# Kernel tuning notes

Hardware: AMD Instinct MI355X
Metric: run time of the kernel (lower is better)

## Reference

```python
import jax, jax.numpy as jnp
import numpy as np
from jax import lax

B, CIN, H, W = 8, 256, 64, 64
CC = 128          # corr_channels
COUT = 64         # out_channels
KH = KW = 5       # corr_kernel_size
SH = SW = 1       # corr_stride
PT, PB = KH // 2, (KH + 1) // 2 - 1   # pad='k'
PL, PR = KW // 2, (KW + 1) // 2 - 1


def setup_inputs() -> dict:
    key = jax.random.key(0)
    k1, k2, k3, k4, k5 = jax.random.split(key, 5)
    x = jax.random.normal(k1, (B, CIN, H, W), dtype=jnp.float32)
    w_ext = jax.random.normal(k2, (CC, CIN, 3, 3), dtype=jnp.float32) * 0.02
    b_ext = jax.random.normal(k3, (CC,), dtype=jnp.float32) * 0.02
    w_reg = jax.random.normal(k4, (COUT, CC, KH, KW), dtype=jnp.float32) * 0.02
    b_reg = jax.random.normal(k5, (COUT,), dtype=jnp.float32) * 0.02
    return {"x": x, "w_ext": w_ext, "b_ext": b_ext, "w_reg": w_reg, "b_reg": b_reg}


def _forward(x, w_ext, b_ext, w_reg, b_reg):
    # feature extraction: 3x3 conv, padding 1
    f = lax.conv_general_dilated(x, w_ext, (1, 1), ((1, 1), (1, 1)))
    f = f + b_ext[None, :, None, None]
    # local autocorrelation: multiply each window element by the window center, per channel
    fp = jnp.pad(f, ((0, 0), (0, 0), (PT, PB), (PL, PR)))
    nH = (fp.shape[2] - KH) // SH + 1
    nW = (fp.shape[3] - KW) // SW + 1
    center = fp[:, :, KH // 2:KH // 2 + nH * SH:SH, KW // 2:KW // 2 + nW * SW:SW]  # [B,CC,nH,nW]
    patches = jnp.stack(
        [fp[:, :, u:u + nH * SH:SH, v:v + nW * SW:SW] for u in range(KH) for v in range(KW)],
        axis=-1)  # [B,CC,nH,nW,KH*KW]
    corr = patches * center[..., None]  # [B,CC,nH,nW,KH*KW]
    out = jnp.einsum('bcijk,ock->bijo', corr, w_reg.reshape(COUT, CC, KH * KW))
    out = out + b_reg
    return out.transpose(0, 3, 1, 2)  # permute=True -> [B, COUT, nH, nW]


def reference(x, w_ext, b_ext, w_reg, b_reg):
    return _forward(x, w_ext, b_ext, w_reg, b_reg)
```

## Files before the change

### kernel.cpp

```cpp
#include <hip/hip_runtime.h>
#include <hip/hip_bf16.h>

#define B_    8
#define CIN_  256
#define CC_   128
#define COUT_ 64
#define HP_   68
#define HPX_  (HP_ * HP_)
#define XQW_  66
#define XQPX_ (XQW_ * XQW_)

typedef __attribute__((ext_vector_type(8))) short bh8;
typedef __attribute__((ext_vector_type(4))) float f4;

__device__ __forceinline__ ushort f2bf(float f) {
    uint u = __float_as_uint(f);
    return (ushort)((u + 0x7fffu + ((u >> 16) & 1u)) >> 16);
}
__device__ __forceinline__ float bf2f(ushort s) {
    return __uint_as_float(((uint)s) << 16);
}
__device__ __forceinline__ short f2bf_c(float f) {
    __hip_bfloat16 h = __float2bfloat16(f);
    short s;
    __builtin_memcpy(&s, &h, 2);
    return s;
}

__global__ __launch_bounds__(256) void zero_ring(ushort* __restrict__ fpad_t) {
    int e = blockIdx.x * 256 + threadIdx.x;
    if (e >= 8 * 528 * 16) return;
    int seg = e & 15;
    int t = e >> 4;
    int b = t / 528, rp = t - b * 528;
    int i, j;
    if (rp < 136) { i = rp / 68; j = rp - (rp / 68) * 68; }
    else if (rp < 272) { int r = rp - 136; i = 66 + r / 68; j = r - (r / 68) * 68; }
    else { int r = rp - 272; i = 2 + (r >> 2); int c = r & 3; j = (c < 2) ? c : c + 64; }
    uint4 z; z.x = 0u; z.y = 0u; z.z = 0u; z.w = 0u;
    *(uint4*)&fpad_t[(((size_t)b * HPX_) + i * HP_ + j) * 128 + seg * 8] = z;
}

__global__ __launch_bounds__(256) void prep_x(const float* __restrict__ x,
                                              ushort* __restrict__ xq) {
    __shared__ float xt[2][32][65];
    const int tid = threadIdx.x;
    const int rp = blockIdx.x, cb = blockIdx.y, b = blockIdx.z;

#pragma unroll
    for (int rr = 0; rr < 2; ++rr) {
        int y = rp * 2 + rr - 1;
        if ((unsigned)y < 64u) {
            int xx = tid & 63, wv = tid >> 6;
#pragma unroll
            for (int it = 0; it < 8; ++it) {
                int ci = it * 4 + wv;
                xt[rr][ci][xx] = x[(((size_t)(b * CIN_ + cb * 32 + ci)) * 64 + y) * 64 + xx];
            }
        }
    }
    __syncthreads();

    for (int e = tid; e < 528; e += 256) {
        int rr = e / 264, t = e - rr * 264;
        int hc = t >> 2, seg = t & 3;
        int y = rp * 2 + rr - 1, xx = hc - 1;
        uint pk[4] = {0u, 0u, 0u, 0u};
        if ((unsigned)y < 64u && (unsigned)xx < 64u) {
#pragma unroll
            for (int i = 0; i < 4; ++i) {
                uint lo = f2bf(xt[rr][seg * 8 + i * 2][xx]);
                uint hi = f2bf(xt[rr][seg * 8 + i * 2 + 1][xx]);
                pk[i] = lo | (hi << 16);
            }
        }
        uint4 v; v.x = pk[0]; v.y = pk[1]; v.z = pk[2]; v.w = pk[3];
        *(uint4*)&xq[((((size_t)(b * 8 + cb)) * XQPX_) + (rp * 2 + rr) * XQW_ + hc) * 32 + seg * 8] = v;
    }
}

__global__ void prep_wext(const float* __restrict__ w, short* __restrict__ wg) {
    int e = blockIdx.x * 256 + threadIdx.x;
    if (e >= 8 * 9 * 128 * 32) return;
    int ci = e & 31;
    int t  = e >> 5;
    int cc = t & 127;
    int t2 = t >> 7;
    int rs = t2 % 9, cb = t2 / 9;
    wg[e] = (short)f2bf(w[(cc * CIN_ + cb * 32 + ci) * 9 + rs]);
}

__global__ void prep_wA(const float* __restrict__ w, short* __restrict__ wa) {
    int e = blockIdx.x * 256 + threadIdx.x;
    if (e >= 4 * 25 * 64 * 32) return;
    int ci = e & 31;
    int o  = (e >> 5) & 63;
    int rest = e >> 11;
    int k = rest % 25, q = rest / 25;
    wa[e] = (short)f2bf(w[(o * CC_ + q * 32 + ci) * 25 + k]);
}

__device__ __forceinline__ void stage_xq(const ushort* __restrict__ xq, short* __restrict__ dst,
                                         int b, int cb, int i0, int j0, int tid) {
    const ushort* base = xq + (((size_t)(b * 8 + cb)) * XQPX_) * 32;
    for (int e = tid; e < 400; e += 256) {
        int hp = e >> 2, seg = e & 3;
        int hr = hp / 10, hc = hp - hr * 10;
        const ushort* src = base + ((size_t)((i0 + hr) * XQW_ + (j0 + hc))) * 32 + seg * 8;
        *(bh8*)&dst[hp * 72 + seg * 8] = *(const bh8*)src;
    }
}

__global__ __launch_bounds__(256) void conv3x3_mfma(const ushort* __restrict__ xq,
                                                    const short* __restrict__ wg,
                                                    const float* __restrict__ bext,
                                                    ushort* __restrict__ fpad_t) {
    __shared__ __align__(16) short xh[2][100 * 72];
    const int tid = threadIdx.x;
    const int lane = tid & 63, wv = tid >> 6;
    const int j0 = blockIdx.x * 8, i0 = blockIdx.y * 8, b = blockIdx.z;
    const int l15 = lane & 15, kg = lane >> 4;
    const int cc0 = wv * 32;

    f4 acc[2][4] = {};

    stage_xq(xq, xh[0], b, 0, i0, j0, tid);
    __syncthreads();

    for (int cb = 0; cb < 8; ++cb) {
        const int buf = cb & 1;
        if (cb < 7) stage_xq(xq, xh[buf ^ 1], b, cb + 1, i0, j0, tid);

        const short* wbase = wg + (size_t)(cb * 9) * 128 * 32;
#pragma unroll
        for (int rs = 0; rs < 9; ++rs) {
            const int r = rs / 3, s = rs % 3;
            bh8 a[2], bb[4];
#pragma unroll
            for (int mm = 0; mm < 2; ++mm)
                a[mm] = *(const bh8*)(wbase + (rs * 128 + cc0 + mm * 16 + l15) * 32 + kg * 8);
#pragma unroll
            for (int nn = 0; nn < 4; ++nn) {
                int px = nn * 16 + l15, pi = px >> 3, pj = px & 7;
                int hidx = (pi + r) * 10 + (pj + s);
                bb[nn] = *(const bh8*)&xh[buf][hidx * 72 + kg * 8];
            }
#pragma unroll
            for (int mm = 0; mm < 2; ++mm)
#pragma unroll
                for (int nn = 0; nn < 4; ++nn)
                    acc[mm][nn] = __builtin_amdgcn_mfma_f32_16x16x32_bf16(
                        a[mm], bb[nn], acc[mm][nn], 0, 0, 0);
        }
        __syncthreads();
    }

#pragma unroll
    for (int mm = 0; mm < 2; ++mm) {
        const int ccb = cc0 + mm * 16 + kg * 4;
        float bv0 = bext[ccb + 0], bv1 = bext[ccb + 1];
        float bv2 = bext[ccb + 2], bv3 = bext[ccb + 3];
#pragma unroll
        for (int nn = 0; nn < 4; ++nn) {
            int px = nn * 16 + l15, pi = px >> 3, pj = px & 7;
            size_t row = (size_t)b * HPX_ + (2 + i0 + pi) * HP_ + (2 + j0 + pj);
            uint lo = (uint)f2bf(acc[mm][nn][0] + bv0) | ((uint)f2bf(acc[mm][nn][1] + bv1) << 16);
            uint hi = (uint)f2bf(acc[mm][nn][2] + bv2) | ((uint)f2bf(acc[mm][nn][3] + bv3) << 16);
            uint2 pk; pk.x = lo; pk.y = hi;
            *(uint2*)&fpad_t[row * 128 + ccb] = pk;
        }
    }
}

__global__ __launch_bounds__(256) void autocorr_mfma(const ushort* __restrict__ ft,
                                                     const short* __restrict__ wA,
                                                     const float* __restrict__ breg,
                                                     float* __restrict__ out) {
    __shared__ __align__(16) short flds[144 * 136];
    const int tid = threadIdx.x;
    const int lane = tid & 63, wv = tid >> 6;
    const int oh = wv >> 1, ph = wv & 1;
    const int j0 = blockIdx.x * 8, i0 = blockIdx.y * 8, b = blockIdx.z;
    const int l15 = lane & 15, kg = lane >> 4;

    for (int e = tid; e < 2304; e += 256) {
        int hp = e >> 4, seg = e & 15;
        int hr = hp / 12, hc = hp - hr * 12;
        const ushort* src = ft + ((size_t)b * HPX_ + (i0 + hr) * HP_ + (j0 + hc)) * 128 + seg * 8;
        *(bh8*)&flds[hp * 136 + seg * 8] = *(const bh8*)src;
    }
    __syncthreads();

    f4 acc[2][2] = {};
    int base_off[2], cen_off[2];
#pragma unroll
    for (int t = 0; t < 2; ++t) {
        int px = ph * 32 + t * 16 + l15;
        int pi = px >> 3, pj = px & 7;
        base_off[t] = (pi * 12 + pj) * 136 + kg * 8;
        cen_off[t]  = ((pi + 2) * 12 + (pj + 2)) * 136 + kg * 8;
    }

#pragma unroll 1
    for (int q = 0; q < 4; ++q) {
        float cen[2][8];
#pragma unroll
        for (int t = 0; t < 2; ++t) {
            bh8 c8 = *(const bh8*)&flds[cen_off[t] + q * 32];
#pragma unroll
            for (int jj = 0; jj < 8; ++jj) cen[t][jj] = bf2f((ushort)c8[jj]);
        }
        const short* wq = wA + q * (25 * 64 * 32);
#pragma unroll
        for (int k = 0; k < 25; ++k) {
            const int u = k / 5, v = k % 5;
            const int koff = (u * 12 + v) * 136;
            bh8 a[2];
#pragma unroll
            for (int mm = 0; mm < 2; ++mm)
                a[mm] = *(const bh8*)(wq + (k * 64 + oh * 32 + mm * 16 + l15) * 32 + kg * 8);
            bh8 bb[2];
#pragma unroll
            for (int t = 0; t < 2; ++t) {
                bh8 s8 = *(const bh8*)&flds[base_off[t] + q * 32 + koff];
#pragma unroll
                for (int jj = 0; jj < 8; ++jj) {
                    float p = bf2f((ushort)s8[jj]) * cen[t][jj];
                    bb[t][jj] = f2bf_c(p);
                }
            }
#pragma unroll
            for (int mm = 0; mm < 2; ++mm)
#pragma unroll
                for (int t = 0; t < 2; ++t)
                    acc[mm][t] = __builtin_amdgcn_mfma_f32_16x16x32_bf16(
                        a[mm], bb[t], acc[mm][t], 0, 0, 0);
        }
    }

#pragma unroll
    for (int mm = 0; mm < 2; ++mm) {
#pragma unroll
        for (int reg = 0; reg < 4; ++reg) {
            int o = oh * 32 + mm * 16 + kg * 4 + reg;
            float bv = breg[o];
#pragma unroll
            for (int t = 0; t < 2; ++t) {
                int px = ph * 32 + t * 16 + l15, pi = px >> 3, pj = px & 7;
                out[(((size_t)(b * COUT_ + o)) * 64 + i0 + pi) * 64 + j0 + pj] =
                    acc[mm][t][reg] + bv;
            }
        }
    }
}

extern "C" void kernel_launch(void* const* d_in, const int* in_sizes, int n_in,
                              void* d_out, int out_size, void* d_ws, size_t ws_size,
                              hipStream_t stream) {
    const float* x     = (const float*)d_in[0];
    const float* w_ext = (const float*)d_in[1];
    const float* b_ext = (const float*)d_in[2];
    const float* w_reg = (const float*)d_in[3];
    const float* b_reg = (const float*)d_in[4];
    float* out = (float*)d_out;

    char* ws = (char*)d_ws;
    const size_t FPADT_BYTES = (size_t)B_ * HPX_ * 128 * 2;
    const size_t WG_BYTES    = (size_t)8 * 9 * 128 * 32 * 2;
    const size_t WA_BYTES    = (size_t)4 * 25 * 64 * 32 * 2;
    ushort* fpad_t = (ushort*)ws;
    short*  wgq    = (short*)(ws + FPADT_BYTES);
    short*  wa     = (short*)(ws + FPADT_BYTES + WG_BYTES);
    ushort* xq     = (ushort*)(ws + FPADT_BYTES + WG_BYTES + WA_BYTES);

    zero_ring<<<(8 * 528 * 16 + 255) / 256, 256, 0, stream>>>(fpad_t);

    dim3 pgrid(33, 8, 8);
    prep_x<<<pgrid, 256, 0, stream>>>(x, xq);
    prep_wext<<<(8 * 9 * 128 * 32 + 255) / 256, 256, 0, stream>>>(w_ext, wgq);
    prep_wA<<<(4 * 25 * 64 * 32 + 255) / 256, 256, 0, stream>>>(w_reg, wa);

    dim3 grid(8, 8, 8);
    conv3x3_mfma<<<grid, 256, 0, stream>>>(xq, wgq, b_ext, fpad_t);
    autocorr_mfma<<<grid, 256, 0, stream>>>(fpad_t, wa, b_reg, out);
}
```

Baseline: 86.95 us.

## Drop LDS staging in conv and autocorr kernels, merge prep kernels

Both MFMA kernels stop staging input tiles into shared memory and instead have each lane read its B operand straight from global/L2. The work is re-split so each wave owns 16 pixels and all output channels, which removes the barriers and LDS traffic. In exchange, overlapping halo reads now go through the caches and each wave loads the full set of weight A fragments. The zero-ring and two weight-conversion kernels are also merged into one launch to cut launch overhead.

```diff
diff --git a/kernel.cpp b/kernel.cpp
--- a/kernel.cpp
+++ b/kernel.cpp
@@ -27,18 +27,42 @@
     return s;
 }
 
-__global__ __launch_bounds__(256) void zero_ring(ushort* __restrict__ fpad_t) {
+__global__ __launch_bounds__(256) void prep_misc(const float* __restrict__ w_ext,
+                                                 const float* __restrict__ w_reg,
+                                                 short* __restrict__ wg,
+                                                 short* __restrict__ wa,
+                                                 ushort* __restrict__ fpad_t) {
     int e = blockIdx.x * 256 + threadIdx.x;
-    if (e >= 8 * 528 * 16) return;
-    int seg = e & 15;
-    int t = e >> 4;
-    int b = t / 528, rp = t - b * 528;
-    int i, j;
-    if (rp < 136) { i = rp / 68; j = rp - (rp / 68) * 68; }
-    else if (rp < 272) { int r = rp - 136; i = 66 + r / 68; j = r - (r / 68) * 68; }
-    else { int r = rp - 272; i = 2 + (r >> 2); int c = r & 3; j = (c < 2) ? c : c + 64; }
-    uint4 z; z.x = 0u; z.y = 0u; z.z = 0u; z.w = 0u;
-    *(uint4*)&fpad_t[(((size_t)b * HPX_) + i * HP_ + j) * 128 + seg * 8] = z;
+    if (e < 67584) {
+        int seg = e & 15;
+        int t = e >> 4;
+        int b = t / 528, rp = t - b * 528;
+        int i, j;
+        if (rp < 136) { i = rp / 68; j = rp - (rp / 68) * 68; }
+        else if (rp < 272) { int r = rp - 136; i = 66 + r / 68; j = r - (r / 68) * 68; }
+        else { int r = rp - 272; i = 2 + (r >> 2); int c = r & 3; j = (c < 2) ? c : c + 64; }
+        uint4 z; z.x = 0u; z.y = 0u; z.z = 0u; z.w = 0u;
+        *(uint4*)&fpad_t[(((size_t)b * HPX_) + i * HP_ + j) * 128 + seg * 8] = z;
+        return;
+    }
+    e -= 67584;
+    if (e < 294912) {
+        int ci = e & 31;
+        int t  = e >> 5;
+        int cc = t & 127;
+        int t2 = t >> 7;
+        int rs = t2 % 9, cb = t2 / 9;
+        wg[e] = (short)f2bf(w_ext[(cc * CIN_ + cb * 32 + ci) * 9 + rs]);
+        return;
+    }
+    e -= 294912;
+    if (e < 204800) {
+        int ci = e & 31;
+        int o  = (e >> 5) & 63;
+        int rest = e >> 11;
+        int k = rest % 25, q = rest / 25;
+        wa[e] = (short)f2bf(w_reg[(o * CC_ + q * 32 + ci) * 25 + k]);
+    }
 }
 
 __global__ __launch_bounds__(256) void prep_x(const float* __restrict__ x,
@@ -79,96 +103,46 @@
     }
 }
 
-__global__ void prep_wext(const float* __restrict__ w, short* __restrict__ wg) {
-    int e = blockIdx.x * 256 + threadIdx.x;
-    if (e >= 8 * 9 * 128 * 32) return;
-    int ci = e & 31;
-    int t  = e >> 5;
-    int cc = t & 127;
-    int t2 = t >> 7;
-    int rs = t2 % 9, cb = t2 / 9;
-    wg[e] = (short)f2bf(w[(cc * CIN_ + cb * 32 + ci) * 9 + rs]);
-}
-
-__global__ void prep_wA(const float* __restrict__ w, short* __restrict__ wa) {
-    int e = blockIdx.x * 256 + threadIdx.x;
-    if (e >= 4 * 25 * 64 * 32) return;
-    int ci = e & 31;
-    int o  = (e >> 5) & 63;
-    int rest = e >> 11;
-    int k = rest % 25, q = rest / 25;
-    wa[e] = (short)f2bf(w[(o * CC_ + q * 32 + ci) * 25 + k]);
-}
-
-__device__ __forceinline__ void stage_xq(const ushort* __restrict__ xq, short* __restrict__ dst,
-                                         int b, int cb, int i0, int j0, int tid) {
-    const ushort* base = xq + (((size_t)(b * 8 + cb)) * XQPX_) * 32;
-    for (int e = tid; e < 400; e += 256) {
-        int hp = e >> 2, seg = e & 3;
-        int hr = hp / 10, hc = hp - hr * 10;
-        const ushort* src = base + ((size_t)((i0 + hr) * XQW_ + (j0 + hc))) * 32 + seg * 8;
-        *(bh8*)&dst[hp * 72 + seg * 8] = *(const bh8*)src;
-    }
-}
-
 __global__ __launch_bounds__(256) void conv3x3_mfma(const ushort* __restrict__ xq,
                                                     const short* __restrict__ wg,
                                                     const float* __restrict__ bext,
                                                     ushort* __restrict__ fpad_t) {
-    __shared__ __align__(16) short xh[2][100 * 72];
     const int tid = threadIdx.x;
     const int lane = tid & 63, wv = tid >> 6;
     const int j0 = blockIdx.x * 8, i0 = blockIdx.y * 8, b = blockIdx.z;
     const int l15 = lane & 15, kg = lane >> 4;
-    const int cc0 = wv * 32;
-
-    f4 acc[2][4] = {};
-
-    stage_xq(xq, xh[0], b, 0, i0, j0, tid);
-    __syncthreads();
+    const int px = wv * 16 + l15, pi = px >> 3, pj = px & 7;
+
+    f4 acc[8] = {};
 
     for (int cb = 0; cb < 8; ++cb) {
-        const int buf = cb & 1;
-        if (cb < 7) stage_xq(xq, xh[buf ^ 1], b, cb + 1, i0, j0, tid);
-
+        const ushort* xb = xq + (((size_t)(b * 8 + cb)) * XQPX_) * 32;
+        const int xbase = ((i0 + pi) * XQW_ + (j0 + pj)) * 32 + kg * 8;
         const short* wbase = wg + (size_t)(cb * 9) * 128 * 32;
 #pragma unroll
         for (int rs = 0; rs < 9; ++rs) {
             const int r = rs / 3, s = rs % 3;
-            bh8 a[2], bb[4];
-#pragma unroll
-            for (int mm = 0; mm < 2; ++mm)
-                a[mm] = *(const bh8*)(wbase + (rs * 128 + cc0 + mm * 16 + l15) * 32 + kg * 8);
-#pragma unroll
-            for (int nn = 0; nn < 4; ++nn) {
-                int px = nn * 16 + l15, pi = px >> 3, pj = px & 7;
-                int hidx = (pi + r) * 10 + (pj + s);
-                bb[nn] = *(const bh8*)&xh[buf][hidx * 72 + kg * 8];
-            }
-#pragma unroll
-            for (int mm = 0; mm < 2; ++mm)
-#pragma unroll
-                for (int nn = 0; nn < 4; ++nn)
-                    acc[mm][nn] = __builtin_amdgcn_mfma_f32_16x16x32_bf16(
-                        a[mm], bb[nn], acc[mm][nn], 0, 0, 0);
-        }
-        __syncthreads();
-    }
-
-#pragma unroll
-    for (int mm = 0; mm < 2; ++mm) {
-        const int ccb = cc0 + mm * 16 + kg * 4;
+            bh8 bb = *(const bh8*)&xb[xbase + (r * XQW_ + s) * 32];
+            bh8 a[8];
+#pragma unroll
+            for (int mm = 0; mm < 8; ++mm)
+                a[mm] = *(const bh8*)(wbase + (rs * 128 + mm * 16 + l15) * 32 + kg * 8);
+#pragma unroll
+            for (int mm = 0; mm < 8; ++mm)
+                acc[mm] = __builtin_amdgcn_mfma_f32_16x16x32_bf16(a[mm], bb, acc[mm], 0, 0, 0);
+        }
+    }
+
+#pragma unroll
+    for (int mm = 0; mm < 8; ++mm) {
+        const int ccb = mm * 16 + kg * 4;
         float bv0 = bext[ccb + 0], bv1 = bext[ccb + 1];
         float bv2 = bext[ccb + 2], bv3 = bext[ccb + 3];
-#pragma unroll
-        for (int nn = 0; nn < 4; ++nn) {
-            int px = nn * 16 + l15, pi = px >> 3, pj = px & 7;
-            size_t row = (size_t)b * HPX_ + (2 + i0 + pi) * HP_ + (2 + j0 + pj);
-            uint lo = (uint)f2bf(acc[mm][nn][0] + bv0) | ((uint)f2bf(acc[mm][nn][1] + bv1) << 16);
-            uint hi = (uint)f2bf(acc[mm][nn][2] + bv2) | ((uint)f2bf(acc[mm][nn][3] + bv3) << 16);
-            uint2 pk; pk.x = lo; pk.y = hi;
-            *(uint2*)&fpad_t[row * 128 + ccb] = pk;
-        }
+        size_t row = (size_t)b * HPX_ + (2 + i0 + pi) * HP_ + (2 + j0 + pj);
+        uint lo = (uint)f2bf(acc[mm][0] + bv0) | ((uint)f2bf(acc[mm][1] + bv1) << 16);
+        uint hi = (uint)f2bf(acc[mm][2] + bv2) | ((uint)f2bf(acc[mm][3] + bv3) << 16);
+        uint2 pk; pk.x = lo; pk.y = hi;
+        *(uint2*)&fpad_t[row * 128 + ccb] = pk;
     }
 }
 
@@ -176,80 +150,50 @@
                                                      const short* __restrict__ wA,
                                                      const float* __restrict__ breg,
                                                      float* __restrict__ out) {
-    __shared__ __align__(16) short flds[144 * 136];
     const int tid = threadIdx.x;
     const int lane = tid & 63, wv = tid >> 6;
-    const int oh = wv >> 1, ph = wv & 1;
     const int j0 = blockIdx.x * 8, i0 = blockIdx.y * 8, b = blockIdx.z;
     const int l15 = lane & 15, kg = lane >> 4;
-
-    for (int e = tid; e < 2304; e += 256) {
-        int hp = e >> 4, seg = e & 15;
-        int hr = hp / 12, hc = hp - hr * 12;
-        const ushort* src = ft + ((size_t)b * HPX_ + (i0 + hr) * HP_ + (j0 + hc)) * 128 + seg * 8;
-        *(bh8*)&flds[hp * 136 + seg * 8] = *(const bh8*)src;
-    }
-    __syncthreads();
-
-    f4 acc[2][2] = {};
-    int base_off[2], cen_off[2];
-#pragma unroll
-    for (int t = 0; t < 2; ++t) {
-        int px = ph * 32 + t * 16 + l15;
-        int pi = px >> 3, pj = px & 7;
-        base_off[t] = (pi * 12 + pj) * 136 + kg * 8;
-        cen_off[t]  = ((pi + 2) * 12 + (pj + 2)) * 136 + kg * 8;
-    }
+    const int px = wv * 16 + l15, pi = px >> 3, pj = px & 7;
+
+    const ushort* fb = ft + (size_t)b * HPX_ * 128;
+    const int base = ((i0 + pi) * HP_ + (j0 + pj)) * 128 + kg * 8;
+
+    f4 acc[4] = {};
 
 #pragma unroll 1
     for (int q = 0; q < 4; ++q) {
-        float cen[2][8];
-#pragma unroll
-        for (int t = 0; t < 2; ++t) {
-            bh8 c8 = *(const bh8*)&flds[cen_off[t] + q * 32];
-#pragma unroll
-            for (int jj = 0; jj < 8; ++jj) cen[t][jj] = bf2f((ushort)c8[jj]);
-        }
+        bh8 c8 = *(const bh8*)&fb[base + (2 * HP_ + 2) * 128 + q * 32];
+        float cen[8];
+#pragma unroll
+        for (int jj = 0; jj < 8; ++jj) cen[jj] = bf2f((ushort)c8[jj]);
+
         const short* wq = wA + q * (25 * 64 * 32);
 #pragma unroll
         for (int k = 0; k < 25; ++k) {
             const int u = k / 5, v = k % 5;
-            const int koff = (u * 12 + v) * 136;
-            bh8 a[2];
-#pragma unroll
-            for (int mm = 0; mm < 2; ++mm)
-                a[mm] = *(const bh8*)(wq + (k * 64 + oh * 32 + mm * 16 + l15) * 32 + kg * 8);
-            bh8 bb[2];
-#pragma unroll
-            for (int t = 0; t < 2; ++t) {
-                bh8 s8 = *(const bh8*)&flds[base_off[t] + q * 32 + koff];
-#pragma unroll
-                for (int jj = 0; jj < 8; ++jj) {
-                    float p = bf2f((ushort)s8[jj]) * cen[t][jj];
-                    bb[t][jj] = f2bf_c(p);
-                }
-            }
-#pragma unroll
-            for (int mm = 0; mm < 2; ++mm)
-#pragma unroll
-                for (int t = 0; t < 2; ++t)
-                    acc[mm][t] = __builtin_amdgcn_mfma_f32_16x16x32_bf16(
-                        a[mm], bb[t], acc[mm][t], 0, 0, 0);
-        }
-    }
-
-#pragma unroll
-    for (int mm = 0; mm < 2; ++mm) {
+            bh8 s8 = *(const bh8*)&fb[base + (u * HP_ + v) * 128 + q * 32];
+            bh8 a[4];
+#pragma unroll
+            for (int mm = 0; mm < 4; ++mm)
+                a[mm] = *(const bh8*)(wq + (k * 64 + mm * 16 + l15) * 32 + kg * 8);
+            bh8 bb;
+#pragma unroll
+            for (int jj = 0; jj < 8; ++jj)
+                bb[jj] = f2bf_c(bf2f((ushort)s8[jj]) * cen[jj]);
+#pragma unroll
+            for (int mm = 0; mm < 4; ++mm)
+                acc[mm] = __builtin_amdgcn_mfma_f32_16x16x32_bf16(a[mm], bb, acc[mm], 0, 0, 0);
+        }
+    }
+
+#pragma unroll
+    for (int mm = 0; mm < 4; ++mm) {
 #pragma unroll
         for (int reg = 0; reg < 4; ++reg) {
-            int o = oh * 32 + mm * 16 + kg * 4 + reg;
-            float bv = breg[o];
-#pragma unroll
-            for (int t = 0; t < 2; ++t) {
-                int px = ph * 32 + t * 16 + l15, pi = px >> 3, pj = px & 7;
-                out[(((size_t)(b * COUT_ + o)) * 64 + i0 + pi) * 64 + j0 + pj] =
-                    acc[mm][t][reg] + bv;
-            }
+            int o = mm * 16 + kg * 4 + reg;
+            out[(((size_t)(b * COUT_ + o)) * 64 + i0 + pi) * 64 + j0 + pj] =
+                acc[mm][reg] + breg[o];
         }
     }
 }
@@ -273,12 +217,11 @@
     short*  wa     = (short*)(ws + FPADT_BYTES + WG_BYTES);
     ushort* xq     = (ushort*)(ws + FPADT_BYTES + WG_BYTES + WA_BYTES);
 
-    zero_ring<<<(8 * 528 * 16 + 255) / 256, 256, 0, stream>>>(fpad_t);
+    const int PREP_TOTAL = 67584 + 294912 + 204800;
+    prep_misc<<<(PREP_TOTAL + 255) / 256, 256, 0, stream>>>(w_ext, w_reg, wgq, wa, fpad_t);
 
     dim3 pgrid(33, 8, 8);
     prep_x<<<pgrid, 256, 0, stream>>>(x, xq);
-    prep_wext<<<(8 * 9 * 128 * 32 + 255) / 256, 256, 0, stream>>>(w_ext, wgq);
-    prep_wA<<<(4 * 25 * 64 * 32 + 255) / 256, 256, 0, stream>>>(w_reg, wa);
 
     dim3 grid(8, 8, 8);
     conv3x3_mfma<<<grid, 256, 0, stream>>>(xq, wgq, b_ext, fpad_t);
```

Measured after the change: 182.1 us. 109% more time.
